# Kernel optimization log

Hardware: AMD Instinct MI355X
Metric: run time of the kernel (lower is better)

Reference implementation:

```python
import jax, jax.numpy as jnp
import numpy as np
import math

D = 256
H = 8
HD = D // H
FF = 1024


def pos2posemb(pos, num_pos_feats=64, temperature=10000.0):
    scale = 2 * math.pi
    pos = pos * scale
    dim_t = jnp.arange(num_pos_feats, dtype=jnp.float32)
    dim_t = temperature ** (2.0 * jnp.floor(dim_t / 2) / num_pos_feats)
    pe = pos[..., None] / dim_t  # [N,4,64]
    pe = jnp.stack((jnp.sin(pe[..., 0::2]), jnp.cos(pe[..., 1::2])), axis=-1)  # [N,4,32,2]
    return pe.reshape(pe.shape[0], -1)  # [N,256]


def layer_norm(x, w, b, eps=1e-5):
    m = jnp.mean(x, axis=-1, keepdims=True)
    v = jnp.mean((x - m) ** 2, axis=-1, keepdims=True)
    return (x - m) * jax.lax.rsqrt(v + eps) * w + b


def setup_inputs() -> dict:
    key = jax.random.key(0)
    ks = jax.random.split(key, 24)
    N = 4096
    s = 0.02
    inp = {
        "ref_pts": jax.random.uniform(ks[0], (N, 4), jnp.float32),
        "pred_boxes": jax.random.uniform(ks[1], (N, 4), jnp.float32),
        "scores": jax.random.uniform(ks[2], (N,), jnp.float32),
        "output_embedding": jax.random.normal(ks[3], (N, D), jnp.float32),
        "query_pos": jax.random.normal(ks[4], (N, D), jnp.float32),
        "group_ids": jax.random.randint(ks[5], (N,), 0, 4, jnp.int64),
        "g_size": 4,
        "in_proj_w": jax.random.normal(ks[6], (3 * D, D), jnp.float32) * s,
        "in_proj_b": jnp.zeros((3 * D,), jnp.float32),
        "out_proj_w": jax.random.normal(ks[7], (D, D), jnp.float32) * s,
        "out_proj_b": jnp.zeros((D,), jnp.float32),
        "lin1_w": jax.random.normal(ks[8], (FF, D), jnp.float32) * s,
        "lin1_b": jnp.zeros((FF,), jnp.float32),
        "lin2_w": jax.random.normal(ks[9], (D, FF), jnp.float32) * s,
        "lin2_b": jnp.zeros((D,), jnp.float32),
        "feat1_w": jax.random.normal(ks[10], (FF, D), jnp.float32) * s,
        "feat1_b": jnp.zeros((FF,), jnp.float32),
        "feat2_w": jax.random.normal(ks[11], (D, FF), jnp.float32) * s,
        "feat2_b": jnp.zeros((D,), jnp.float32),
        "norm1_w": jnp.ones((D,), jnp.float32),
        "norm1_b": jnp.zeros((D,), jnp.float32),
        "norm2_w": jnp.ones((D,), jnp.float32),
        "norm2_b": jnp.zeros((D,), jnp.float32),
        "normf_w": jnp.ones((D,), jnp.float32),
        "normf_b": jnp.zeros((D,), jnp.float32),
    }
    return inp


def reference(ref_pts, pred_boxes, scores, output_embedding, query_pos,
              in_proj_w, in_proj_b, out_proj_w, out_proj_b,
              lin1_w, lin1_b, lin2_w, lin2_b,
              feat1_w, feat1_b, feat2_w, feat2_b,
              norm1_w, norm1_b, norm2_w, norm2_b, normf_w, normf_b,
              group_ids, g_size):
    N = ref_pts.shape[0]
    is_pos = scores > 0.5  # score_thr = 0.5
    # ref_pts[is_pos] = pred_boxes.detach()[is_pos]
    ref = jnp.where(is_pos[:, None], jax.lax.stop_gradient(pred_boxes), ref_pts)

    out_embed = output_embedding
    qpos_emb = pos2posemb(ref)  # [N,256]
    qk = qpos_emb + out_embed

    # grouped block-diagonal mask: 0 within same group, -inf across groups
    mask = jnp.where(group_ids[:, None] == group_ids[None, :], 0.0, -jnp.inf)

    # MultiheadAttention (eval, dropout=0)
    q = qk @ in_proj_w[:D].T + in_proj_b[:D]
    k = qk @ in_proj_w[D:2 * D].T + in_proj_b[D:2 * D]
    v = out_embed @ in_proj_w[2 * D:].T + in_proj_b[2 * D:]
    qh = q.reshape(N, H, HD)
    kh = k.reshape(N, H, HD)
    vh = v.reshape(N, H, HD)
    logits = jnp.einsum("nhd,mhd->hnm", qh, kh) / jnp.sqrt(jnp.float32(HD)) + mask
    attn = jax.nn.softmax(logits, axis=-1)
    ctx = jnp.einsum("hnm,mhd->nhd", attn, vh).reshape(N, D)
    tgt2 = ctx @ out_proj_w.T + out_proj_b

    tgt = layer_norm(out_embed + tgt2, norm1_w, norm1_b)
    ffn = jax.nn.relu(tgt @ lin1_w.T + lin1_b) @ lin2_w.T + lin2_b
    tgt = layer_norm(tgt + ffn, norm2_w, norm2_b)

    feat = jax.nn.relu(tgt @ feat1_w.T + feat1_b) @ feat2_w.T + feat2_b
    query_feat = layer_norm(query_pos + feat, normf_w, normf_b)

    # query_pos[is_pos] = query_feat[is_pos]
    query_pos_out = jnp.where(is_pos[:, None], query_feat, query_pos)
    return query_pos_out
```

## Files before the change

### kernel.cpp

```cpp
#include <hip/hip_runtime.h>


typedef __attribute__((ext_vector_type(8))) __bf16 bf16x8;
typedef __attribute__((ext_vector_type(4))) float f32x4;

#define NSPLIT 2

static __device__ __forceinline__ unsigned short f2bf(float f) {
    union { float f; unsigned u; } v; v.f = f;
    unsigned r = v.u + 0x7fffu + ((v.u >> 16) & 1u);
    return (unsigned short)(r >> 16);
}

__global__ __launch_bounds__(1024) void k_sort(
    const int* __restrict__ gid, int N,
    int* __restrict__ perm, int* __restrict__ rank,
    int* __restrict__ gid_s, int* __restrict__ offs)
{
    __shared__ int cnt[1024][4];
    __shared__ int base[4];
    int t = threadIdx.x;
    int per = N / 1024;
    int c[4] = {0, 0, 0, 0};
    for (int i = 0; i < per; ++i) c[gid[t * per + i] & 3]++;
    for (int g = 0; g < 4; ++g) cnt[t][g] = c[g];
    __syncthreads();
    for (int off = 1; off < 1024; off <<= 1) {
        int v[4] = {0, 0, 0, 0};
        if (t >= off) for (int g = 0; g < 4; ++g) v[g] = cnt[t - off][g];
        __syncthreads();
        if (t >= off) for (int g = 0; g < 4; ++g) cnt[t][g] += v[g];
        __syncthreads();
    }
    if (t == 0) {
        base[0] = 0;
        base[1] = cnt[1023][0];
        base[2] = base[1] + cnt[1023][1];
        base[3] = base[2] + cnt[1023][2];
        offs[0] = 0; offs[1] = base[1]; offs[2] = base[2]; offs[3] = base[3]; offs[4] = N;
    }
    __syncthreads();
    int run[4];
    for (int g = 0; g < 4; ++g) run[g] = base[g] + (t ? cnt[t - 1][g] : 0);
    for (int i = 0; i < per; ++i) {
        int n = t * per + i;
        int g = gid[n] & 3;
        int p = run[g]++;
        perm[p] = n; rank[n] = p; gid_s[p] = g;
    }
}

__global__ __launch_bounds__(256) void k_prep(
    const float* __restrict__ ref_pts, const float* __restrict__ pred_boxes,
    const float* __restrict__ scores, const float* __restrict__ embed,
    const float* __restrict__ qpos, const int* __restrict__ rank,
    unsigned short* __restrict__ qk_bf, unsigned short* __restrict__ emb_bf,
    float* __restrict__ emb_f32s, float* __restrict__ qpos_s)
{
    int n = blockIdx.x, d = threadIdx.x;
    int pos = rank[n];
    bool ip = scores[n] > 0.5f;
    int c = d >> 6, k = (d >> 1) & 31, s = d & 1;
    float p = (ip ? pred_boxes : ref_pts)[n * 4 + c] * 6.283185307179586f;
    float freq = exp2f(-(float)k * (13.287712379549449f / 32.0f));
    float ang = p * freq;
    float e = s ? cosf(ang) : sinf(ang);
    float em = embed[(size_t)n * 256 + d];
    qk_bf[(size_t)pos * 256 + d] = f2bf(e + em);
    emb_bf[(size_t)pos * 256 + d] = f2bf(em);
    emb_f32s[(size_t)pos * 256 + d] = em;
    qpos_s[(size_t)pos * 256 + d] = qpos[(size_t)n * 256 + d];
}

__global__ __launch_bounds__(256) void k_convw(
    const float* __restrict__ w0, const float* __restrict__ w1,
    const float* __restrict__ w2, const float* __restrict__ w3,
    const float* __restrict__ w4, const float* __restrict__ w5,
    unsigned short* __restrict__ o0, unsigned short* __restrict__ o1,
    unsigned short* __restrict__ o2, unsigned short* __restrict__ o3,
    unsigned short* __restrict__ o4, unsigned short* __restrict__ o5)
{
    long i = ((long)blockIdx.x * 256 + threadIdx.x) * 4;
    const float* src; unsigned short* dst; long off;
    if      (i <  196608) { src = w0; dst = o0; off = i; }
    else if (i <  262144) { src = w1; dst = o1; off = i -  196608; }
    else if (i <  524288) { src = w2; dst = o2; off = i -  262144; }
    else if (i <  786432) { src = w3; dst = o3; off = i -  524288; }
    else if (i < 1048576) { src = w4; dst = o4; off = i -  786432; }
    else                  { src = w5; dst = o5; off = i - 1048576; }
    float4 v = *(const float4*)(src + off);
    ushort4 o; o.x = f2bf(v.x); o.y = f2bf(v.y); o.z = f2bf(v.z); o.w = f2bf(v.w);
    *(ushort4*)(dst + off) = o;
}

#define EPI_QKV     0
#define EPI_RESF32  2
#define EPI_RELUBF  3

template<int EPI>
__global__ __launch_bounds__(256) void k_gemm(
    const unsigned short* __restrict__ A, const unsigned short* __restrict__ A2,
    const unsigned short* __restrict__ B,
    const float* __restrict__ bias, const float* __restrict__ resid,
    void* __restrict__ out, void* __restrict__ out2,
    int M, int Nout, int K)
{
    __shared__ __align__(16) unsigned short As[2][64][72];
    __shared__ __align__(16) unsigned short Bs[2][64][72];
    int mt = M >> 6;
    int bm = blockIdx.x % mt, bn = blockIdx.x / mt;
    int m0 = bm * 64, c0 = bn * 64;
    int tid = threadIdx.x;
    int wave = tid >> 6, lane = tid & 63;
    int wr = wave >> 1, wc = wave & 1;
    int g = lane >> 4, r15 = lane & 15;

    const unsigned short* Asrc = A;
    if constexpr (EPI == EPI_QKV) { if (c0 >= 512) Asrc = A2; }

    int r0 = tid >> 3, u0 = tid & 7;
    int r1 = (tid + 256) >> 3, u1 = tid & 7;

    const unsigned short* Abase = Asrc + (size_t)m0 * K;
    const unsigned short* Bbase = B + (size_t)c0 * K;

    uint4 a0 = *(const uint4*)(Abase + (size_t)r0 * K + u0 * 8);
    uint4 a1 = *(const uint4*)(Abase + (size_t)r1 * K + u1 * 8);
    uint4 b0 = *(const uint4*)(Bbase + (size_t)r0 * K + u0 * 8);
    uint4 b1 = *(const uint4*)(Bbase + (size_t)r1 * K + u1 * 8);
    *(uint4*)(&As[0][r0][u0 * 8]) = a0;
    *(uint4*)(&As[0][r1][u1 * 8]) = a1;
    *(uint4*)(&Bs[0][r0][u0 * 8]) = b0;
    *(uint4*)(&Bs[0][r1][u1 * 8]) = b1;
    __syncthreads();

    f32x4 acc[2][2] = {};
    int nk = K >> 6;
    for (int kt = 0; kt < nk; ++kt) {
        int cur = kt & 1;
        bool more = (kt + 1 < nk);
        if (more) {
            int kc = (kt + 1) << 6;
            a0 = *(const uint4*)(Abase + (size_t)r0 * K + kc + u0 * 8);
            a1 = *(const uint4*)(Abase + (size_t)r1 * K + kc + u1 * 8);
            b0 = *(const uint4*)(Bbase + (size_t)r0 * K + kc + u0 * 8);
            b1 = *(const uint4*)(Bbase + (size_t)r1 * K + kc + u1 * 8);
        }
        #pragma unroll
        for (int kk = 0; kk < 2; ++kk) {
            bf16x8 af0 = *(const bf16x8*)(&As[cur][wr * 32 + r15][kk * 32 + g * 8]);
            bf16x8 af1 = *(const bf16x8*)(&As[cur][wr * 32 + 16 + r15][kk * 32 + g * 8]);
            bf16x8 bf0 = *(const bf16x8*)(&Bs[cur][wc * 32 + r15][kk * 32 + g * 8]);
            bf16x8 bf1 = *(const bf16x8*)(&Bs[cur][wc * 32 + 16 + r15][kk * 32 + g * 8]);
            acc[0][0] = __builtin_amdgcn_mfma_f32_16x16x32_bf16(af0, bf0, acc[0][0], 0, 0, 0);
            acc[0][1] = __builtin_amdgcn_mfma_f32_16x16x32_bf16(af0, bf1, acc[0][1], 0, 0, 0);
            acc[1][0] = __builtin_amdgcn_mfma_f32_16x16x32_bf16(af1, bf0, acc[1][0], 0, 0, 0);
            acc[1][1] = __builtin_amdgcn_mfma_f32_16x16x32_bf16(af1, bf1, acc[1][1], 0, 0, 0);
        }
        if (more) {
            *(uint4*)(&As[cur ^ 1][r0][u0 * 8]) = a0;
            *(uint4*)(&As[cur ^ 1][r1][u1 * 8]) = a1;
            *(uint4*)(&Bs[cur ^ 1][r0][u0 * 8]) = b0;
            *(uint4*)(&Bs[cur ^ 1][r1][u1 * 8]) = b1;
            __syncthreads();
        }
    }

    #pragma unroll
    for (int ti = 0; ti < 2; ++ti)
    #pragma unroll
    for (int tj = 0; tj < 2; ++tj)
    #pragma unroll
    for (int r = 0; r < 4; ++r) {
        int n = m0 + wr * 32 + ti * 16 + g * 4 + r;
        int o = c0 + wc * 32 + tj * 16 + r15;
        float v = acc[ti][tj][r] + bias[o];
        if constexpr (EPI == EPI_QKV) {
            if (o < 512) {
                float s = (o < 256) ? (0.17677669529663687f * 1.4426950408889634f) : 1.0f;
                ((unsigned short*)out)[(size_t)n * 512 + o] = f2bf(v * s);
            } else {
                ((unsigned short*)out2)[(size_t)(o - 512) * M + n] = f2bf(v);
            }
        } else if constexpr (EPI == EPI_RESF32) {
            ((float*)out)[(size_t)n * Nout + o] = v + resid[(size_t)n * Nout + o];
        } else {
            ((unsigned short*)out)[(size_t)n * Nout + o] = f2bf(fmaxf(v, 0.0f));
        }
    }
}

__global__ __launch_bounds__(256) void k_attn(
    const unsigned short* __restrict__ QK, const unsigned short* __restrict__ Vt,
    const int* __restrict__ gid_s, const int* __restrict__ offs,
    float* __restrict__ Opart, float* __restrict__ lpart, int N)
{
    __shared__ __align__(16) unsigned short Ks[2][64][40];
    __shared__ __align__(16) unsigned short Vs[2][32][72];
    __shared__ __align__(16) unsigned short Ps[4][16][64];
    __shared__ __align__(16) int gks[2][64];

    int qtiles = N >> 6;
    int bid = blockIdx.x;
    int qt = bid % qtiles;
    int hs = bid / qtiles;
    int h = hs & 7;
    int sp = hs >> 3;
    int q0 = qt * 64;
    int tid = threadIdx.x, wave = tid >> 6, lane = tid & 63;
    int g = lane >> 4, r15 = lane & 15;
    int n0 = q0 + wave * 16;

    int g_lo = gid_s[q0], g_hi = gid_s[q0 + 63];
    int tlo = offs[g_lo] >> 6;
    int thi = (offs[g_hi + 1] + 63) >> 6;
    int ntiles = thi - tlo;
    int chunk = (ntiles + NSPLIT - 1) / NSPLIT;
    int t0 = tlo + sp * chunk;
    int t1 = min(t0 + chunk, thi);

    if (t0 >= t1) {
        #pragma unroll
        for (int r = 0; r < 4; ++r) {
            int n = n0 + g * 4 + r;
            Opart[((size_t)sp * N + n) * 256 + h * 32 + r15] = 0.f;
            Opart[((size_t)sp * N + n) * 256 + h * 32 + 16 + r15] = 0.f;
        }
        if (g == 0) lpart[((size_t)sp * N + n0 + r15) * 8 + h] = 0.f;
        return;
    }

    bf16x8 qf = *(const bf16x8*)(QK + (size_t)(n0 + r15) * 512 + h * 32 + g * 8);
    int gq = gid_s[n0 + r15];

    int kr_ = tid >> 2, kc_ = (tid & 3) * 8;
    int vd_ = tid >> 3, vc_ = (tid & 7) * 8;

    f32x4 O0 = {}, O1 = {};
    float lloc = 0.f;
    unsigned short* PsW = &Ps[wave][0][0];

    {
        int m0 = t0 << 6;
        *(uint4*)(&Ks[0][kr_][kc_]) = *(const uint4*)(QK + (size_t)(m0 + kr_) * 512 + 256 + h * 32 + kc_);
        *(uint4*)(&Vs[0][vd_][vc_]) = *(const uint4*)(Vt + (size_t)(h * 32 + vd_) * N + m0 + vc_);
        if (tid < 64) gks[0][tid] = gid_s[m0 + tid];
    }
    __syncthreads();

    int cur = 0;
    for (int t = t0; t < t1; ++t) {
        bool more = (t + 1 < t1);
        uint4 kn, vn; int gn = 0;
        if (more) {
            int m0n = (t + 1) << 6;
            kn = *(const uint4*)(QK + (size_t)(m0n + kr_) * 512 + 256 + h * 32 + kc_);
            vn = *(const uint4*)(Vt + (size_t)(h * 32 + vd_) * N + m0n + vc_);
            if (tid < 64) gn = gid_s[m0n + tid];
        }

        f32x4 S[4];
        #pragma unroll
        for (int t_ = 0; t_ < 4; ++t_) {
            bf16x8 kf = *(const bf16x8*)(&Ks[cur][t_ * 16 + r15][g * 8]);
            f32x4 z = {};
            S[t_] = __builtin_amdgcn_mfma_f32_16x16x32_bf16(kf, qf, z, 0, 0, 0);
        }
        #pragma unroll
        for (int t_ = 0; t_ < 4; ++t_) {
            int4 g4 = *(const int4*)(&gks[cur][t_ * 16 + g * 4]);
            float p0 = (g4.x == gq) ? exp2f(S[t_][0]) : 0.f;
            float p1 = (g4.y == gq) ? exp2f(S[t_][1]) : 0.f;
            float p2 = (g4.z == gq) ? exp2f(S[t_][2]) : 0.f;
            float p3 = (g4.w == gq) ? exp2f(S[t_][3]) : 0.f;
            lloc += (p0 + p1) + (p2 + p3);
            ushort4 pw;
            pw.x = f2bf(p0); pw.y = f2bf(p1); pw.z = f2bf(p2); pw.w = f2bf(p3);
            int off = t_ * 32 + g * 8;
            int byte = r15 * 128 + ((((off >> 4) ^ (r15 & 7)) << 4) | (off & 15));
            *(ushort4*)((char*)PsW + byte) = pw;
        }
        #pragma unroll
        for (int kk = 0; kk < 2; ++kk) {
            int byte = r15 * 128 + (((kk * 4 + g) ^ (r15 & 7)) << 4);
            bf16x8 pf = *(const bf16x8*)((char*)PsW + byte);
            bf16x8 v0 = *(const bf16x8*)(&Vs[cur][r15][kk * 32 + g * 8]);
            bf16x8 v1 = *(const bf16x8*)(&Vs[cur][16 + r15][kk * 32 + g * 8]);
            O0 = __builtin_amdgcn_mfma_f32_16x16x32_bf16(pf, v0, O0, 0, 0, 0);
            O1 = __builtin_amdgcn_mfma_f32_16x16x32_bf16(pf, v1, O1, 0, 0, 0);
        }

        if (more) {
            *(uint4*)(&Ks[cur ^ 1][kr_][kc_]) = kn;
            *(uint4*)(&Vs[cur ^ 1][vd_][vc_]) = vn;
            if (tid < 64) gks[cur ^ 1][tid] = gn;
        }
        __syncthreads();
        cur ^= 1;
    }

    float l = lloc;
    l += __shfl_xor(l, 16, 64);
    l += __shfl_xor(l, 32, 64);
    if (g == 0) lpart[((size_t)sp * N + n0 + r15) * 8 + h] = l;

    #pragma unroll
    for (int r = 0; r < 4; ++r) {
        int n = n0 + g * 4 + r;
        Opart[((size_t)sp * N + n) * 256 + h * 32 + r15]      = O0[r];
        Opart[((size_t)sp * N + n) * 256 + h * 32 + 16 + r15] = O1[r];
    }
}

__global__ __launch_bounds__(256) void k_comb(
    const float* __restrict__ Opart, const float* __restrict__ lpart,
    unsigned short* __restrict__ ctx, int N)
{
    int n = blockIdx.x, d = threadIdx.x;
    int h = d >> 5;
    float l0 = lpart[((size_t)n) * 8 + h];
    float l1 = lpart[((size_t)N + n) * 8 + h];
    float inv = 1.0f / (l0 + l1);
    float o = Opart[(size_t)n * 256 + d] + Opart[((size_t)N + n) * 256 + d];
    ctx[(size_t)n * 256 + d] = f2bf(o * inv);
}

template<int MODE>
__global__ __launch_bounds__(256) void k_ln(
    const float* __restrict__ y, const float* __restrict__ w, const float* __restrict__ b,
    float* __restrict__ of32, unsigned short* __restrict__ obf,
    const float* __restrict__ scores, const float* __restrict__ qpos_s,
    const int* __restrict__ perm)
{
    int wave = threadIdx.x >> 6, lane = threadIdx.x & 63;
    int row = blockIdx.x * 4 + wave;
    const float4 x = *(const float4*)(y + (size_t)row * 256 + lane * 4);
    float s = x.x + x.y + x.z + x.w;
    #pragma unroll
    for (int off = 1; off < 64; off <<= 1) s += __shfl_xor(s, off, 64);
    float mean = s * (1.0f / 256.0f);
    float d0 = x.x - mean, d1 = x.y - mean, d2 = x.z - mean, d3 = x.w - mean;
    float q = d0 * d0 + d1 * d1 + d2 * d2 + d3 * d3;
    #pragma unroll
    for (int off = 1; off < 64; off <<= 1) q += __shfl_xor(q, off, 64);
    float rs = rsqrtf(q * (1.0f / 256.0f) + 1e-5f);
    const float4 wv = *(const float4*)(w + lane * 4);
    const float4 bv = *(const float4*)(b + lane * 4);
    float o0 = d0 * rs * wv.x + bv.x;
    float o1 = d1 * rs * wv.y + bv.y;
    float o2 = d2 * rs * wv.z + bv.z;
    float o3 = d3 * rs * wv.w + bv.w;
    if constexpr (MODE == 0) {
        *(float4*)(of32 + (size_t)row * 256 + lane * 4) = make_float4(o0, o1, o2, o3);
        ushort4 ob; ob.x = f2bf(o0); ob.y = f2bf(o1); ob.z = f2bf(o2); ob.w = f2bf(o3);
        *(ushort4*)(obf + (size_t)row * 256 + lane * 4) = ob;
    } else if constexpr (MODE == 1) {
        ushort4 ob; ob.x = f2bf(o0); ob.y = f2bf(o1); ob.z = f2bf(o2); ob.w = f2bf(o3);
        *(ushort4*)(obf + (size_t)row * 256 + lane * 4) = ob;
    } else {
        int n = perm[row];
        bool ip = scores[n] > 0.5f;
        const float4 qp = *(const float4*)(qpos_s + (size_t)row * 256 + lane * 4);
        float4 ov = ip ? make_float4(o0, o1, o2, o3) : qp;
        *(float4*)(of32 + (size_t)n * 256 + lane * 4) = ov;
    }
}

extern "C" void kernel_launch(void* const* d_in, const int* in_sizes, int n_in,
                              void* d_out, int out_size, void* d_ws, size_t ws_size,
                              hipStream_t stream)
{
    const float* ref_pts    = (const float*)d_in[0];
    const float* pred_boxes = (const float*)d_in[1];
    const float* scores     = (const float*)d_in[2];
    const float* out_embed  = (const float*)d_in[3];
    const float* query_pos  = (const float*)d_in[4];
    const int*   group_ids  = (const int*)d_in[5];
    const float* in_proj_w  = (const float*)d_in[7];
    const float* in_proj_b  = (const float*)d_in[8];
    const float* out_proj_w = (const float*)d_in[9];
    const float* out_proj_b = (const float*)d_in[10];
    const float* lin1_w     = (const float*)d_in[11];
    const float* lin1_b     = (const float*)d_in[12];
    const float* lin2_w     = (const float*)d_in[13];
    const float* lin2_b     = (const float*)d_in[14];
    const float* feat1_w    = (const float*)d_in[15];
    const float* feat1_b    = (const float*)d_in[16];
    const float* feat2_w    = (const float*)d_in[17];
    const float* feat2_b    = (const float*)d_in[18];
    const float* norm1_w    = (const float*)d_in[19];
    const float* norm1_b    = (const float*)d_in[20];
    const float* norm2_w    = (const float*)d_in[21];
    const float* norm2_b    = (const float*)d_in[22];
    const float* normf_w    = (const float*)d_in[23];
    const float* normf_b    = (const float*)d_in[24];

    const int N = in_sizes[2];

    char* ws = (char*)d_ws;
    size_t off = 0;
    auto alloc = [&](size_t bytes) -> void* {
        void* p = ws + off; off += (bytes + 255) & ~(size_t)255; return p;
    };
    unsigned short* wqkv   = (unsigned short*)alloc((size_t)768 * 256 * 2);
    unsigned short* wout   = (unsigned short*)alloc((size_t)256 * 256 * 2);
    unsigned short* wlin1  = (unsigned short*)alloc((size_t)1024 * 256 * 2);
    unsigned short* wlin2  = (unsigned short*)alloc((size_t)256 * 1024 * 2);
    unsigned short* wfeat1 = (unsigned short*)alloc((size_t)1024 * 256 * 2);
    unsigned short* wfeat2 = (unsigned short*)alloc((size_t)256 * 1024 * 2);
    unsigned short* qk_bf  = (unsigned short*)alloc((size_t)N * 256 * 2);
    unsigned short* emb_bf = (unsigned short*)alloc((size_t)N * 256 * 2);
    unsigned short* QKbuf  = (unsigned short*)alloc((size_t)N * 512 * 2);
    unsigned short* Vtbuf  = (unsigned short*)alloc((size_t)256 * N * 2);
    unsigned short* ctxbuf = (unsigned short*)alloc((size_t)N * 256 * 2);
    float*          ybuf   = (float*)alloc((size_t)N * 256 * 4);
    float*          tgtf   = (float*)alloc((size_t)N * 256 * 4);
    unsigned short* tgtbf  = (unsigned short*)alloc((size_t)N * 256 * 2);
    unsigned short* t2bf   = (unsigned short*)alloc((size_t)N * 256 * 2);
    unsigned short* hbuf   = (unsigned short*)alloc((size_t)N * 1024 * 2);
    float* emb_f32s = (float*)alloc((size_t)N * 256 * 4);
    float* qpos_s   = (float*)alloc((size_t)N * 256 * 4);
    int* permbuf = (int*)alloc((size_t)N * 4);
    int* rankbuf = (int*)alloc((size_t)N * 4);
    int* gidsbuf = (int*)alloc((size_t)N * 4);
    int* offsbuf = (int*)alloc(32 * 4);
    float* Opartbuf = (float*)alloc((size_t)NSPLIT * N * 256 * 4);
    float* lbuf     = (float*)alloc((size_t)NSPLIT * N * 8 * 4);
    (void)ws_size; (void)n_in; (void)out_size;

    const int mt = N >> 6;

    k_sort<<<1, 1024, 0, stream>>>(group_ids, N, permbuf, rankbuf, gidsbuf, offsbuf);
    k_convw<<<1280, 256, 0, stream>>>(in_proj_w, out_proj_w, lin1_w, lin2_w, feat1_w, feat2_w,
                                      wqkv, wout, wlin1, wlin2, wfeat1, wfeat2);
    k_prep<<<N, 256, 0, stream>>>(ref_pts, pred_boxes, scores, out_embed, query_pos, rankbuf,
                                  qk_bf, emb_bf, emb_f32s, qpos_s);

    k_gemm<EPI_QKV><<<mt * 12, 256, 0, stream>>>(
        qk_bf, emb_bf, wqkv, in_proj_b, nullptr, QKbuf, Vtbuf, N, 768, 256);

    k_attn<<<mt * 8 * NSPLIT, 256, 0, stream>>>(QKbuf, Vtbuf, gidsbuf, offsbuf,
                                                Opartbuf, lbuf, N);
    k_comb<<<N, 256, 0, stream>>>(Opartbuf, lbuf, ctxbuf, N);

    k_gemm<EPI_RESF32><<<mt * 4, 256, 0, stream>>>(
        ctxbuf, nullptr, wout, out_proj_b, emb_f32s, ybuf, nullptr, N, 256, 256);
    k_ln<0><<<N / 4, 256, 0, stream>>>(ybuf, norm1_w, norm1_b, tgtf, tgtbf, nullptr, nullptr, nullptr);

    k_gemm<EPI_RELUBF><<<mt * 16, 256, 0, stream>>>(
        tgtbf, nullptr, wlin1, lin1_b, nullptr, hbuf, nullptr, N, 1024, 256);
    k_gemm<EPI_RESF32><<<mt * 4, 256, 0, stream>>>(
        hbuf, nullptr, wlin2, lin2_b, tgtf, ybuf, nullptr, N, 256, 1024);
    k_ln<1><<<N / 4, 256, 0, stream>>>(ybuf, norm2_w, norm2_b, nullptr, t2bf, nullptr, nullptr, nullptr);

    k_gemm<EPI_RELUBF><<<mt * 16, 256, 0, stream>>>(
        t2bf, nullptr, wfeat1, feat1_b, nullptr, hbuf, nullptr, N, 1024, 256);
    k_gemm<EPI_RESF32><<<mt * 4, 256, 0, stream>>>(
        hbuf, nullptr, wfeat2, feat2_b, qpos_s, ybuf, nullptr, N, 256, 1024);
    k_ln<2><<<N / 4, 256, 0, stream>>>(ybuf, normf_w, normf_b, (float*)d_out, nullptr,
                                       scores, qpos_s, permbuf);
}
```

Measured before the change: 123.1 us.

## Fuse attention combine and LayerNorm into full-row GEMMs, merge setup kernels

Merges weight conversion and group sorting into one launch, folds the split-attention combine into the out-projection GEMM's A-tile load, and fuses bias, residual and LayerNorm (plus final scatter/select) into new 64x256-tile GEMM kernels. This removes the k_comb and k_ln launches and the fp32 intermediate buffer round trips. The fused GEMMs launch only one block per 64 rows, which greatly reduces parallelism on a large GPU.

```diff
diff --git a/kernel.cpp b/kernel.cpp
--- a/kernel.cpp
+++ b/kernel.cpp
@@ -12,11 +12,31 @@
     return (unsigned short)(r >> 16);
 }
 
-__global__ __launch_bounds__(1024) void k_sort(
+__global__ __launch_bounds__(1024) void k_setup(
+    const float* __restrict__ w0, const float* __restrict__ w1,
+    const float* __restrict__ w2, const float* __restrict__ w3,
+    const float* __restrict__ w4, const float* __restrict__ w5,
+    unsigned short* __restrict__ o0, unsigned short* __restrict__ o1,
+    unsigned short* __restrict__ o2, unsigned short* __restrict__ o3,
+    unsigned short* __restrict__ o4, unsigned short* __restrict__ o5,
     const int* __restrict__ gid, int N,
     int* __restrict__ perm, int* __restrict__ rank,
     int* __restrict__ gid_s, int* __restrict__ offs)
 {
+    if (blockIdx.x < 320) {
+        long i = ((long)blockIdx.x * 1024 + threadIdx.x) * 4;
+        const float* src; unsigned short* dst; long off;
+        if      (i <  196608) { src = w0; dst = o0; off = i; }
+        else if (i <  262144) { src = w1; dst = o1; off = i -  196608; }
+        else if (i <  524288) { src = w2; dst = o2; off = i -  262144; }
+        else if (i <  786432) { src = w3; dst = o3; off = i -  524288; }
+        else if (i < 1048576) { src = w4; dst = o4; off = i -  786432; }
+        else                  { src = w5; dst = o5; off = i - 1048576; }
+        float4 v = *(const float4*)(src + off);
+        ushort4 o; o.x = f2bf(v.x); o.y = f2bf(v.y); o.z = f2bf(v.z); o.w = f2bf(v.w);
+        *(ushort4*)(dst + off) = o;
+        return;
+    }
     __shared__ int cnt[1024][4];
     __shared__ int base[4];
     int t = threadIdx.x;
@@ -55,7 +75,8 @@
     const float* __restrict__ scores, const float* __restrict__ embed,
     const float* __restrict__ qpos, const int* __restrict__ rank,
     unsigned short* __restrict__ qk_bf, unsigned short* __restrict__ emb_bf,
-    float* __restrict__ emb_f32s, float* __restrict__ qpos_s)
+    float* __restrict__ emb_f32s, float* __restrict__ qpos_s,
+    float* __restrict__ scores_s)
 {
     int n = blockIdx.x, d = threadIdx.x;
     int pos = rank[n];
@@ -70,38 +91,17 @@
     emb_bf[(size_t)pos * 256 + d] = f2bf(em);
     emb_f32s[(size_t)pos * 256 + d] = em;
     qpos_s[(size_t)pos * 256 + d] = qpos[(size_t)n * 256 + d];
-}
-
-__global__ __launch_bounds__(256) void k_convw(
-    const float* __restrict__ w0, const float* __restrict__ w1,
-    const float* __restrict__ w2, const float* __restrict__ w3,
-    const float* __restrict__ w4, const float* __restrict__ w5,
-    unsigned short* __restrict__ o0, unsigned short* __restrict__ o1,
-    unsigned short* __restrict__ o2, unsigned short* __restrict__ o3,
-    unsigned short* __restrict__ o4, unsigned short* __restrict__ o5)
-{
-    long i = ((long)blockIdx.x * 256 + threadIdx.x) * 4;
-    const float* src; unsigned short* dst; long off;
-    if      (i <  196608) { src = w0; dst = o0; off = i; }
-    else if (i <  262144) { src = w1; dst = o1; off = i -  196608; }
-    else if (i <  524288) { src = w2; dst = o2; off = i -  262144; }
-    else if (i <  786432) { src = w3; dst = o3; off = i -  524288; }
-    else if (i < 1048576) { src = w4; dst = o4; off = i -  786432; }
-    else                  { src = w5; dst = o5; off = i - 1048576; }
-    float4 v = *(const float4*)(src + off);
-    ushort4 o; o.x = f2bf(v.x); o.y = f2bf(v.y); o.z = f2bf(v.z); o.w = f2bf(v.w);
-    *(ushort4*)(dst + off) = o;
+    if (d == 0) scores_s[pos] = scores[n];
 }
 
 #define EPI_QKV     0
-#define EPI_RESF32  2
 #define EPI_RELUBF  3
 
 template<int EPI>
 __global__ __launch_bounds__(256) void k_gemm(
     const unsigned short* __restrict__ A, const unsigned short* __restrict__ A2,
     const unsigned short* __restrict__ B,
-    const float* __restrict__ bias, const float* __restrict__ resid,
+    const float* __restrict__ bias,
     void* __restrict__ out, void* __restrict__ out2,
     int M, int Nout, int K)
 {
@@ -119,7 +119,7 @@
     if constexpr (EPI == EPI_QKV) { if (c0 >= 512) Asrc = A2; }
 
     int r0 = tid >> 3, u0 = tid & 7;
-    int r1 = (tid + 256) >> 3, u1 = tid & 7;
+    int r1 = 32 + (tid >> 3), u1 = tid & 7;
 
     const unsigned short* Abase = Asrc + (size_t)m0 * K;
     const unsigned short* Bbase = B + (size_t)c0 * K;
@@ -182,10 +182,171 @@
             } else {
                 ((unsigned short*)out2)[(size_t)(o - 512) * M + n] = f2bf(v);
             }
-        } else if constexpr (EPI == EPI_RESF32) {
-            ((float*)out)[(size_t)n * Nout + o] = v + resid[(size_t)n * Nout + o];
         } else {
             ((unsigned short*)out)[(size_t)n * Nout + o] = f2bf(fmaxf(v, 0.0f));
+        }
+    }
+}
+
+template<int K, int MODE>
+__global__ __launch_bounds__(256) void k_gemmln(
+    const unsigned short* __restrict__ Abf,
+    const float* __restrict__ Opart, const float* __restrict__ lpart,
+    const unsigned short* __restrict__ Bw,
+    const float* __restrict__ bias, const float* __restrict__ resid,
+    const float* __restrict__ lnw, const float* __restrict__ lnb,
+    float* __restrict__ outf32, unsigned short* __restrict__ outbf,
+    const float* __restrict__ scores_s, const int* __restrict__ perm, int N)
+{
+    __shared__ __align__(16) unsigned short As[2][64][72];
+    __shared__ __align__(16) unsigned short Bs[2][256][72];
+    __shared__ float sW[64][65];
+    __shared__ float qW[64][65];
+    __shared__ float mS[64], rS[64];
+
+    const int m0 = blockIdx.x * 64;
+    const int tid = threadIdx.x, wave = tid >> 6, lane = tid & 63;
+    const int g = lane >> 4, r15 = lane & 15;
+
+    const int ar0 = tid >> 3, ar1 = 32 + (tid >> 3), au = tid & 7;
+    int bR[8];
+    #pragma unroll
+    for (int i = 0; i < 8; ++i) bR[i] = i * 32 + (tid >> 3);
+
+    auto loadA = [&](int kt, int r) -> uint4 {
+        int n = m0 + r;
+        int c = kt * 64 + au * 8;
+        if constexpr (MODE == 0) {
+            int h = c >> 5;
+            float l0 = lpart[(size_t)n * 8 + h];
+            float l1 = lpart[((size_t)N + n) * 8 + h];
+            float inv = 1.0f / (l0 + l1);
+            const float* p0 = Opart + (size_t)n * 256 + c;
+            const float* p1 = Opart + ((size_t)N + n) * 256 + c;
+            float4 x0 = *(const float4*)(p0);
+            float4 x1 = *(const float4*)(p0 + 4);
+            float4 y0 = *(const float4*)(p1);
+            float4 y1 = *(const float4*)(p1 + 4);
+            unsigned e0 = f2bf((x0.x + y0.x) * inv) | ((unsigned)f2bf((x0.y + y0.y) * inv) << 16);
+            unsigned e1 = f2bf((x0.z + y0.z) * inv) | ((unsigned)f2bf((x0.w + y0.w) * inv) << 16);
+            unsigned e2 = f2bf((x1.x + y1.x) * inv) | ((unsigned)f2bf((x1.y + y1.y) * inv) << 16);
+            unsigned e3 = f2bf((x1.z + y1.z) * inv) | ((unsigned)f2bf((x1.w + y1.w) * inv) << 16);
+            uint4 o; o.x = e0; o.y = e1; o.z = e2; o.w = e3;
+            return o;
+        } else {
+            return *(const uint4*)(Abf + (size_t)n * K + c);
+        }
+    };
+
+    uint4 pa0 = loadA(0, ar0);
+    uint4 pa1 = loadA(0, ar1);
+    uint4 pb[8];
+    #pragma unroll
+    for (int i = 0; i < 8; ++i)
+        pb[i] = *(const uint4*)(Bw + (size_t)bR[i] * K + au * 8);
+    *(uint4*)(&As[0][ar0][au * 8]) = pa0;
+    *(uint4*)(&As[0][ar1][au * 8]) = pa1;
+    #pragma unroll
+    for (int i = 0; i < 8; ++i)
+        *(uint4*)(&Bs[0][bR[i]][au * 8]) = pb[i];
+    __syncthreads();
+
+    f32x4 acc[4][4] = {};
+    constexpr int nk = K >> 6;
+    for (int kt = 0; kt < nk; ++kt) {
+        int cur = kt & 1;
+        bool more = (kt + 1 < nk);
+        if (more) {
+            int kc = (kt + 1) << 6;
+            pa0 = loadA(kt + 1, ar0);
+            pa1 = loadA(kt + 1, ar1);
+            #pragma unroll
+            for (int i = 0; i < 8; ++i)
+                pb[i] = *(const uint4*)(Bw + (size_t)bR[i] * K + kc + au * 8);
+        }
+        #pragma unroll
+        for (int kk = 0; kk < 2; ++kk) {
+            bf16x8 af[4], bfr[4];
+            #pragma unroll
+            for (int ti = 0; ti < 4; ++ti)
+                af[ti] = *(const bf16x8*)(&As[cur][ti * 16 + r15][kk * 32 + g * 8]);
+            #pragma unroll
+            for (int tj = 0; tj < 4; ++tj)
+                bfr[tj] = *(const bf16x8*)(&Bs[cur][wave * 64 + tj * 16 + r15][kk * 32 + g * 8]);
+            #pragma unroll
+            for (int ti = 0; ti < 4; ++ti)
+                #pragma unroll
+                for (int tj = 0; tj < 4; ++tj)
+                    acc[ti][tj] = __builtin_amdgcn_mfma_f32_16x16x32_bf16(af[ti], bfr[tj], acc[ti][tj], 0, 0, 0);
+        }
+        if (more) {
+            *(uint4*)(&As[cur ^ 1][ar0][au * 8]) = pa0;
+            *(uint4*)(&As[cur ^ 1][ar1][au * 8]) = pa1;
+            #pragma unroll
+            for (int i = 0; i < 8; ++i)
+                *(uint4*)(&Bs[cur ^ 1][bR[i]][au * 8]) = pb[i];
+            __syncthreads();
+        }
+    }
+
+    float sp_[4][4] = {}, qp_[4][4] = {};
+    #pragma unroll
+    for (int ti = 0; ti < 4; ++ti)
+    #pragma unroll
+    for (int tj = 0; tj < 4; ++tj)
+    #pragma unroll
+    for (int r = 0; r < 4; ++r) {
+        int n = ti * 16 + g * 4 + r;
+        int col = wave * 64 + tj * 16 + r15;
+        float v = acc[ti][tj][r] + bias[col] + resid[(size_t)(m0 + n) * 256 + col];
+        acc[ti][tj][r] = v;
+        sp_[ti][r] += v;
+        qp_[ti][r] += v * v;
+    }
+    #pragma unroll
+    for (int ti = 0; ti < 4; ++ti)
+    #pragma unroll
+    for (int r = 0; r < 4; ++r) {
+        int n = ti * 16 + g * 4 + r;
+        sW[n][wave * 16 + r15] = sp_[ti][r];
+        qW[n][wave * 16 + r15] = qp_[ti][r];
+    }
+    __syncthreads();
+    {
+        int n = tid >> 2, seg = tid & 3;
+        float s = 0.f, q = 0.f;
+        #pragma unroll
+        for (int j = 0; j < 16; ++j) { s += sW[n][seg * 16 + j]; q += qW[n][seg * 16 + j]; }
+        s += __shfl_xor(s, 1, 64); s += __shfl_xor(s, 2, 64);
+        q += __shfl_xor(q, 1, 64); q += __shfl_xor(q, 2, 64);
+        if (seg == 0) {
+            float mean = s * (1.0f / 256.0f);
+            float var = q * (1.0f / 256.0f) - mean * mean;
+            mS[n] = mean;
+            rS[n] = rsqrtf(fmaxf(var, 0.f) + 1e-5f);
+        }
+    }
+    __syncthreads();
+
+    #pragma unroll
+    for (int ti = 0; ti < 4; ++ti)
+    #pragma unroll
+    for (int tj = 0; tj < 4; ++tj)
+    #pragma unroll
+    for (int r = 0; r < 4; ++r) {
+        int n = ti * 16 + g * 4 + r;
+        int col = wave * 64 + tj * 16 + r15;
+        float o = (acc[ti][tj][r] - mS[n]) * rS[n] * lnw[col] + lnb[col];
+        if constexpr (MODE == 0) {
+            outf32[(size_t)(m0 + n) * 256 + col] = o;
+            outbf[(size_t)(m0 + n) * 256 + col] = f2bf(o);
+        } else if constexpr (MODE == 1) {
+            outbf[(size_t)(m0 + n) * 256 + col] = f2bf(o);
+        } else {
+            bool ip = scores_s[m0 + n] > 0.5f;
+            float qp = resid[(size_t)(m0 + n) * 256 + col];
+            int no = perm[m0 + n];
+            outf32[(size_t)no * 256 + col] = ip ? o : qp;
         }
     }
 }
@@ -309,60 +470,6 @@
         int n = n0 + g * 4 + r;
         Opart[((size_t)sp * N + n) * 256 + h * 32 + r15]      = O0[r];
         Opart[((size_t)sp * N + n) * 256 + h * 32 + 16 + r15] = O1[r];
-    }
-}
-
-__global__ __launch_bounds__(256) void k_comb(
-    const float* __restrict__ Opart, const float* __restrict__ lpart,
-    unsigned short* __restrict__ ctx, int N)
-{
-    int n = blockIdx.x, d = threadIdx.x;
-    int h = d >> 5;
-    float l0 = lpart[((size_t)n) * 8 + h];
-    float l1 = lpart[((size_t)N + n) * 8 + h];
-    float inv = 1.0f / (l0 + l1);
-    float o = Opart[(size_t)n * 256 + d] + Opart[((size_t)N + n) * 256 + d];
-    ctx[(size_t)n * 256 + d] = f2bf(o * inv);
-}
-
-template<int MODE>
-__global__ __launch_bounds__(256) void k_ln(
-    const float* __restrict__ y, const float* __restrict__ w, const float* __restrict__ b,
-    float* __restrict__ of32, unsigned short* __restrict__ obf,
-    const float* __restrict__ scores, const float* __restrict__ qpos_s,
-    const int* __restrict__ perm)
-{
-    int wave = threadIdx.x >> 6, lane = threadIdx.x & 63;
-    int row = blockIdx.x * 4 + wave;
-    const float4 x = *(const float4*)(y + (size_t)row * 256 + lane * 4);
-    float s = x.x + x.y + x.z + x.w;
-    #pragma unroll
-    for (int off = 1; off < 64; off <<= 1) s += __shfl_xor(s, off, 64);
-    float mean = s * (1.0f / 256.0f);
-    float d0 = x.x - mean, d1 = x.y - mean, d2 = x.z - mean, d3 = x.w - mean;
-    float q = d0 * d0 + d1 * d1 + d2 * d2 + d3 * d3;
-    #pragma unroll
-    for (int off = 1; off < 64; off <<= 1) q += __shfl_xor(q, off, 64);
-    float rs = rsqrtf(q * (1.0f / 256.0f) + 1e-5f);
-    const float4 wv = *(const float4*)(w + lane * 4);
-    const float4 bv = *(const float4*)(b + lane * 4);
-    float o0 = d0 * rs * wv.x + bv.x;
-    float o1 = d1 * rs * wv.y + bv.y;
-    float o2 = d2 * rs * wv.z + bv.z;
-    float o3 = d3 * rs * wv.w + bv.w;
-    if constexpr (MODE == 0) {
-        *(float4*)(of32 + (size_t)row * 256 + lane * 4) = make_float4(o0, o1, o2, o3);
-        ushort4 ob; ob.x = f2bf(o0); ob.y = f2bf(o1); ob.z = f2bf(o2); ob.w = f2bf(o3);
-        *(ushort4*)(obf + (size_t)row * 256 + lane * 4) = ob;
-    } else if constexpr (MODE == 1) {
-        ushort4 ob; ob.x = f2bf(o0); ob.y = f2bf(o1); ob.z = f2bf(o2); ob.w = f2bf(o3);
-        *(ushort4*)(obf + (size_t)row * 256 + lane * 4) = ob;
-    } else {
-        int n = perm[row];
-        bool ip = scores[n] > 0.5f;
-        const float4 qp = *(const float4*)(qpos_s + (size_t)row * 256 + lane * 4);
-        float4 ov = ip ? make_float4(o0, o1, o2, o3) : qp;
-        *(float4*)(of32 + (size_t)n * 256 + lane * 4) = ov;
     }
 }
 
@@ -412,14 +519,13 @@
     unsigned short* emb_bf = (unsigned short*)alloc((size_t)N * 256 * 2);
     unsigned short* QKbuf  = (unsigned short*)alloc((size_t)N * 512 * 2);
     unsigned short* Vtbuf  = (unsigned short*)alloc((size_t)256 * N * 2);
-    unsigned short* ctxbuf = (unsigned short*)alloc((size_t)N * 256 * 2);
-    float*          ybuf   = (float*)alloc((size_t)N * 256 * 4);
     float*          tgtf   = (float*)alloc((size_t)N * 256 * 4);
     unsigned short* tgtbf  = (unsigned short*)alloc((size_t)N * 256 * 2);
     unsigned short* t2bf   = (unsigned short*)alloc((size_t)N * 256 * 2);
     unsigned short* hbuf   = (unsigned short*)alloc((size_t)N * 1024 * 2);
     float* emb_f32s = (float*)alloc((size_t)N * 256 * 4);
     float* qpos_s   = (float*)alloc((size_t)N * 256 * 4);
+    float* scores_s = (float*)alloc((size_t)N * 4);
     int* permbuf = (int*)alloc((size_t)N * 4);
     int* rankbuf = (int*)alloc((size_t)N * 4);
     int* gidsbuf = (int*)alloc((size_t)N * 4);
@@ -430,33 +536,26 @@
 
     const int mt = N >> 6;
 
-    k_sort<<<1, 1024, 0, stream>>>(group_ids, N, permbuf, rankbuf, gidsbuf, offsbuf);
-    k_convw<<<1280, 256, 0, stream>>>(in_proj_w, out_proj_w, lin1_w, lin2_w, feat1_w, feat2_w,
-                                      wqkv, wout, wlin1, wlin2, wfeat1, wfeat2);
+    k_setup<<<321, 1024, 0, stream>>>(in_proj_w, out_proj_w, lin1_w, lin2_w, feat1_w, feat2_w,
+                                      wqkv, wout, wlin1, wlin2, wfeat1, wfeat2,
+                                      group_ids, N, permbuf, rankbuf, gidsbuf, offsbuf);
     k_prep<<<N, 256, 0, stream>>>(ref_pts, pred_boxes, scores, out_embed, query_pos, rankbuf,
-                                  qk_bf, emb_bf, emb_f32s, qpos_s);
-
+                                  qk_bf, emb_bf, emb_f32s, qpos_s, scores_s);
     k_gemm<EPI_QKV><<<mt * 12, 256, 0, stream>>>(
-        qk_bf, emb_bf, wqkv, in_proj_b, nullptr, QKbuf, Vtbuf, N, 768, 256);
-
+        qk_bf, emb_bf, wqkv, in_proj_b, QKbuf, Vtbuf, N, 768, 256);
     k_attn<<<mt * 8 * NSPLIT, 256, 0, stream>>>(QKbuf, Vtbuf, gidsbuf, offsbuf,
                                                 Opartbuf, lbuf, N);
-    k_comb<<<N, 256, 0, stream>>>(Opartbuf, lbuf, ctxbuf, N);
-
-    k_gemm<EPI_RESF32><<<mt * 4, 256, 0, stream>>>(
-        ctxbuf, nullptr, wout, out_proj_b, emb_f32s, ybuf, nullptr, N, 256, 256);
-    k_ln<0><<<N / 4, 256, 0, stream>>>(ybuf, norm1_w, norm1_b, tgtf, tgtbf, nullptr, nullptr, nullptr);
-
+    k_gemmln<256, 0><<<mt, 256, 0, stream>>>(
+        nullptr, Opartbuf, lbuf, wout, out_proj_b, emb_f32s,
+        norm1_w, norm1_b, tgtf, tgtbf, nullptr, nullptr, N);
     k_gemm<EPI_RELUBF><<<mt * 16, 256, 0, stream>>>(
-        tgtbf, nullptr, wlin1, lin1_b, nullptr, hbuf, nullptr, N, 1024, 256);
-    k_gemm<EPI_RESF32><<<mt * 4, 256, 0, stream>>>(
-        hbuf, nullptr, wlin2, lin2_b, tgtf, ybuf, nullptr, N, 256, 1024);
-    k_ln<1><<<N / 4, 256, 0, stream>>>(ybuf, norm2_w, norm2_b, nullptr, t2bf, nullptr, nullptr, nullptr);
-
+        tgtbf, nullptr, wlin1, lin1_b, hbuf, nullptr, N, 1024, 256);
+    k_gemmln<1024, 1><<<mt, 256, 0, stream>>>(
+        hbuf, nullptr, nullptr, wlin2, lin2_b, tgtf,
+        norm2_w, norm2_b, nullptr, t2bf, nullptr, nullptr, N);
     k_gemm<EPI_RELUBF><<<mt * 16, 256, 0, stream>>>(
-        t2bf, nullptr, wfeat1, feat1_b, nullptr, hbuf, nullptr, N, 1024, 256);
-    k_gemm<EPI_RESF32><<<mt * 4, 256, 0, stream>>>(
-        hbuf, nullptr, wfeat2, feat2_b, qpos_s, ybuf, nullptr, N, 256, 1024);
-    k_ln<2><<<N / 4, 256, 0, stream>>>(ybuf, normf_w, normf_b, (float*)d_out, nullptr,
-                                       scores, qpos_s, permbuf);
-}
+        t2bf, nullptr, wfeat1, feat1_b, hbuf, nullptr, N, 1024, 256);
+    k_gemmln<1024, 2><<<mt, 256, 0, stream>>>(
+        hbuf, nullptr, nullptr, wfeat2, feat2_b, qpos_s,
+        normf_w, normf_b, (float*)d_out, nullptr, scores_s, permbuf, N);
+}
```

New measurement: 135.0 us. +9.7%, slower.
